# Performance work log

Hardware: AMD Instinct MI355X
Metric: run time of the kernel (lower is better)

## Reference

```python
import jax, jax.numpy as jnp
import numpy as np

B, S, D, HEADS = 2, 1024, 1024, 16
DK = D // HEADS           # 64: size of the 'heads' axis after split (namedtensor quirk)
LOW = D // DK             # 16: size of the contracted 'lower' axis
SCALE = float(D)          # Attention(p, scale=d_model) -> divide by d_model
NEG = -1.0e9


def setup_inputs() -> dict:
    key = jax.random.key(0)
    ks = jax.random.split(key, 8)
    query = jax.random.normal(ks[0], (B, S, D), dtype=jnp.float32)
    key_t = jax.random.normal(ks[1], (B, S, D), dtype=jnp.float32)
    value = jax.random.normal(ks[2], (B, S, D), dtype=jnp.float32)
    mask = jax.random.bernoulli(ks[3], 0.25, (B, S, S))  # True -> masked out
    std = 1.0 / np.sqrt(D)
    Wq = jax.random.normal(ks[4], (D, D), dtype=jnp.float32) * std
    Wk = jax.random.normal(ks[5], (D, D), dtype=jnp.float32) * std
    Wv = jax.random.normal(ks[6], (D, D), dtype=jnp.float32) * std
    Wo = jax.random.normal(ks[7], (D, D), dtype=jnp.float32) * std
    return {"query": query, "key": key_t, "value": value, "mask": mask,
            "Wq": Wq, "Wk": Wk, "Wv": Wv, "Wo": Wo}


def reference(query, key, value, mask, Wq, Wk, Wv, Wo):
    # nn.Linear(d_model, d_model, bias=False): y = x @ W.T
    def split(x, W):
        y = jnp.einsum('bsd,ed->bse', x, W)
        return y.reshape(B, -1, DK, LOW)  # hidden -> ('heads'=DK, 'lower'=LOW)

    q = split(query, Wq)   # [B,Sq,H,L] with H=DK, L=LOW
    k = split(key, Wk)     # [B,Sk,H,L]
    v = split(value, Wv)   # [B,Sk,H,L]

    # scores = query.dot('lower', key) / d_model  -> contract the LOW axis
    scores = jnp.einsum('bqhl,bkhl->bhqk', q, k) / SCALE
    scores = jnp.where(mask[:, None, :, :], NEG, scores)  # scores[mask] = -1e9
    p_attn = jax.nn.softmax(scores, axis=-1)  # softmax over keys; dropout=eval

    # value.dot('keys', p_attn) -> [B,H,L,Q]; stack ('heads','lower') -> hidden
    x = jnp.einsum('bkhl,bhqk->bqhl', v, p_attn).reshape(B, -1, D)
    return jnp.einsum('bsd,ed->bse', x, Wo)
```

## Files before the change

### kernel.cpp

```cpp
#include <hip/hip_runtime.h>
#include <hip/hip_bf16.h>


typedef __hip_bfloat16 bf16;
typedef __attribute__((ext_vector_type(8))) short short8;
typedef __attribute__((ext_vector_type(4))) float f32x4;
typedef __attribute__((ext_vector_type(16))) float f32x16;

__device__ __forceinline__ unsigned short f2bf(float f) {
  union { float f; unsigned u; } x; x.f = f;
  unsigned r = x.u + 0x7FFFu + ((x.u >> 16) & 1u);
  return (unsigned short)(r >> 16);
}

__device__ __forceinline__ unsigned cvt_pk_bf16(float lo, float hi) {
  unsigned r;
  asm("v_cvt_pk_bf16_f32 %0, %1, %2" : "=v"(r) : "v"(lo), "v"(hi));
  return r;
}

__device__ __forceinline__ float fast_exp2(float x) {
#if __has_builtin(__builtin_amdgcn_exp2f)
  return __builtin_amdgcn_exp2f(x);
#else
  return __expf(x * 0.6931471805599453f);
#endif
}

__device__ __forceinline__ void gload16(const void* g, void* l) {
#if __has_builtin(__builtin_amdgcn_global_load_lds)
  __builtin_amdgcn_global_load_lds(
      (const __attribute__((address_space(1))) unsigned*)g,
      (__attribute__((address_space(3))) unsigned*)l, 16, 0, 0);
#else
  *(uint4*)l = *(const uint4*)g;
#endif
}

__global__ void detect_mask(const unsigned char* __restrict__ m, int* __restrict__ flag) {
  const int i = blockIdx.x * 256 + threadIdx.x;
  const uchar4* p = (const uchar4*)m + (size_t)i * 4;
  unsigned any = 0;
#pragma unroll
  for (int j = 0; j < 4; ++j) { uchar4 v = p[j]; any |= (unsigned)v.y | (unsigned)v.z | (unsigned)v.w; }
  if (__ballot(any != 0)) { if ((threadIdx.x & 63) == 0) atomicOr(flag, 1); }
}

__global__ void bitpack_mask(const unsigned char* __restrict__ mB, const int* __restrict__ mI,
                             const int* __restrict__ flag, unsigned* __restrict__ out) {
  const int widx = blockIdx.x * 256 + threadIdx.x;
  const int row = widx >> 5, kb = widx & 31;
  unsigned bits = 0;
  if (*flag) {
    const uchar4* p = (const uchar4*)(mB + (size_t)row * 1024 + kb * 32);
#pragma unroll
    for (int j = 0; j < 8; ++j) {
      uchar4 v = p[j];
      bits |= ((unsigned)(v.x != 0) << (4 * j)) | ((unsigned)(v.y != 0) << (4 * j + 1))
            | ((unsigned)(v.z != 0) << (4 * j + 2)) | ((unsigned)(v.w != 0) << (4 * j + 3));
    }
  } else {
    const int4* p = (const int4*)(mI + (size_t)row * 1024 + kb * 32);
#pragma unroll
    for (int j = 0; j < 8; ++j) {
      int4 v = p[j];
      bits |= ((unsigned)(v.x != 0) << (4 * j)) | ((unsigned)(v.y != 0) << (4 * j + 1))
            | ((unsigned)(v.z != 0) << (4 * j + 2)) | ((unsigned)(v.w != 0) << (4 * j + 3));
    }
  }
  const int bq = row >> 10, qb = (row & 1023) >> 5, qr = row & 31;
  out[((((bq * 32 + qb) * 8 + (kb >> 2)) * 32 + qr) << 2) + (kb & 3)] = bits;
}

__global__ void convert_all(
    const float* __restrict__ s0, const float* __restrict__ s1, const float* __restrict__ s2,
    const float* __restrict__ s3, const float* __restrict__ s4, const float* __restrict__ s5,
    const float* __restrict__ s6,
    bf16* __restrict__ d0, bf16* __restrict__ d1, bf16* __restrict__ d2,
    bf16* __restrict__ d3, bf16* __restrict__ d4, bf16* __restrict__ d5,
    bf16* __restrict__ d6) {
  const int z = blockIdx.y;
  const float* s; bf16* d; int n8; float sc = 1.0f;
  if      (z == 0) { s = s0; d = d0; n8 = 262144; }
  else if (z == 1) { s = s1; d = d1; n8 = 262144; }
  else if (z == 2) { s = s2; d = d2; n8 = 262144; }
  else if (z == 3) { s = s3; d = d3; n8 = 131072; sc = 0.0014088818758681283f; }
  else if (z == 4) { s = s4; d = d4; n8 = 131072; }
  else if (z == 5) { s = s5; d = d5; n8 = 131072; }
  else             { s = s6; d = d6; n8 = 131072; }
  const int i = blockIdx.x * 256 + threadIdx.x;
  if (i >= n8) return;
  const f32x4* p = (const f32x4*)s + (size_t)i * 2;
  f32x4 a = p[0], b = p[1];
  uint4 o;
  o.x = cvt_pk_bf16(a[0] * sc, a[1] * sc); o.y = cvt_pk_bf16(a[2] * sc, a[3] * sc);
  o.z = cvt_pk_bf16(b[0] * sc, b[1] * sc); o.w = cvt_pk_bf16(b[2] * sc, b[3] * sc);
  ((uint4*)d)[i] = o;
}

#define GSTR 40

__global__ __launch_bounds__(256) void gemm_qkv(
    const bf16* __restrict__ A0, const bf16* __restrict__ A1, const bf16* __restrict__ A2,
    const bf16* __restrict__ W0, const bf16* __restrict__ W1, const bf16* __restrict__ W2,
    bf16* __restrict__ C0, bf16* __restrict__ C1, bf16* __restrict__ C2) {
  __shared__ __align__(16) bf16 smem[64 * 136];
  bf16* As = smem;
  bf16* Bs = smem + 4096;
  const int z = blockIdx.z;
  const bf16* __restrict__ A = (z == 0) ? A0 : (z == 1) ? A1 : A2;
  const bf16* __restrict__ W = (z == 0) ? W0 : (z == 1) ? W1 : W2;
  bf16* __restrict__ C = (z == 0) ? C0 : (z == 1) ? C1 : C2;
  const int tid = threadIdx.x, lane = tid & 63, w = tid >> 6;
  const int wr = (w >> 1) * 64, wc = (w & 1) * 32;
  const int row0 = blockIdx.y * 128, col0 = blockIdx.x * 64;
  const int l15 = lane & 15, kg = lane >> 4;

  const int srow = lane >> 2, scol = (lane & 3) * 8;
  const bf16* Ag0 = A + (size_t)(row0 + w * 32 + srow) * 1024 + scol;
  const bf16* Ag1 = A + (size_t)(row0 + w * 32 + 16 + srow) * 1024 + scol;
  const bf16* Bg0 = W + (size_t)(col0 + w * 16 + srow) * 1024 + scol;
  bf16* Al0 = As + w * 1024 + lane * 8;
  bf16* Al1 = As + w * 1024 + 512 + lane * 8;
  bf16* Bl0 = Bs + w * 512 + lane * 8;

  f32x4 acc[4][2];
#pragma unroll
  for (int m = 0; m < 4; ++m)
#pragma unroll
    for (int n = 0; n < 2; ++n)
#pragma unroll
      for (int j = 0; j < 4; ++j) acc[m][n][j] = 0.f;

  for (int t = 0; t < 32; ++t) {
    const int k0 = t * 32;
    gload16(Ag0 + k0, Al0);
    gload16(Ag1 + k0, Al1);
    gload16(Bg0 + k0, Bl0);
    __syncthreads();
    short8 af[4], bfr[2];
#pragma unroll
    for (int m = 0; m < 4; ++m) af[m] = *(const short8*)(&As[(wr + m * 16 + l15) * 32 + kg * 8]);
#pragma unroll
    for (int n = 0; n < 2; ++n) bfr[n] = *(const short8*)(&Bs[(wc + n * 16 + l15) * 32 + kg * 8]);
#pragma unroll
    for (int m = 0; m < 4; ++m)
#pragma unroll
      for (int n = 0; n < 2; ++n)
        acc[m][n] = __builtin_amdgcn_mfma_f32_16x16x32_bf16(af[m], bfr[n], acc[m][n], 0, 0, 0);
    __syncthreads();
  }

  const int bb = row0 >> 10, srel0 = row0 & 1023;
  if (z == 2) {
    bf16* T = smem;
#pragma unroll
    for (int m = 0; m < 4; ++m)
#pragma unroll
      for (int n = 0; n < 2; ++n) {
        const int e = wc + n * 16 + l15;
        const int rb = wr + m * 16 + kg * 4;
        uint2 u;
        u.x = cvt_pk_bf16(acc[m][n][0], acc[m][n][1]);
        u.y = cvt_pk_bf16(acc[m][n][2], acc[m][n][3]);
        *(uint2*)(T + e * 136 + rb) = u;
      }
    __syncthreads();
#pragma unroll
    for (int i = 0; i < 4; ++i) {
      const int idx = i * 256 + tid;
      const int tile = idx >> 6, within = idx & 63;
      const int hl = tile >> 2, kbl = tile & 3;
      const int e_sub = within >> 2, kq4 = within & 3;
      uint4 v = *(const uint4*)(T + (hl * 16 + e_sub) * 136 + kbl * 32 + kq4 * 8);
      const int h = (col0 >> 4) + hl;
      const size_t kb = (size_t)((srel0 >> 5) + kbl);
      *(uint4*)((unsigned short*)C + (((size_t)(bb * 64 + h) * 32 + kb) * 512 + e_sub * 32 + kq4 * 8)) = v;
    }
  } else if (z == 1) {
#pragma unroll
    for (int m = 0; m < 4; ++m)
#pragma unroll
      for (int n = 0; n < 2; ++n) {
        const int ecol = wc + n * 16 + l15;
        const int h = (col0 >> 4) + (ecol >> 4), d = ecol & 15;
#pragma unroll
        for (int j = 0; j < 4; ++j) {
          const int s = srel0 + wr + m * 16 + kg * 4 + j;
          ((unsigned short*)C)[((size_t)(bb * 64 + h) * 32 + (s >> 5)) * 512 + (s & 31) * 16 + d] =
              f2bf(acc[m][n][j]);
        }
      }
  } else {
#pragma unroll
    for (int m = 0; m < 4; ++m)
#pragma unroll
      for (int n = 0; n < 2; ++n) {
        const int col = col0 + wc + n * 16 + l15;
#pragma unroll
        for (int j = 0; j < 4; ++j) {
          const int row = row0 + wr + m * 16 + kg * 4 + j;
          ((unsigned short*)C)[(size_t)row * 1024 + col] = f2bf(acc[m][n][j]);
        }
      }
  }
}

__global__ __launch_bounds__(256) void gemm_out(
    const bf16* __restrict__ A, const bf16* __restrict__ W, float* __restrict__ C) {
  __shared__ __align__(16) bf16 smem[6144];
  bf16* As = smem;
  bf16* Bs = smem + 4096;
  const int tid = threadIdx.x, lane = tid & 63, w = tid >> 6;
  const int wr = (w >> 1) * 64, wc = (w & 1) * 32;
  const int row0 = blockIdx.y * 128, col0 = blockIdx.x * 64;
  const int l15 = lane & 15, kg = lane >> 4;

  const int srow = lane >> 2, scol = (lane & 3) * 8;
  const bf16* Ag0 = A + (size_t)(row0 + w * 32 + srow) * 1024 + scol;
  const bf16* Ag1 = A + (size_t)(row0 + w * 32 + 16 + srow) * 1024 + scol;
  const bf16* Bg0 = W + (size_t)(col0 + w * 16 + srow) * 1024 + scol;
  bf16* Al0 = As + w * 1024 + lane * 8;
  bf16* Al1 = As + w * 1024 + 512 + lane * 8;
  bf16* Bl0 = Bs + w * 512 + lane * 8;

  f32x4 acc[4][2];
#pragma unroll
  for (int m = 0; m < 4; ++m)
#pragma unroll
    for (int n = 0; n < 2; ++n)
#pragma unroll
      for (int j = 0; j < 4; ++j) acc[m][n][j] = 0.f;

  for (int t = 0; t < 32; ++t) {
    const int k0 = t * 32;
    gload16(Ag0 + k0, Al0);
    gload16(Ag1 + k0, Al1);
    gload16(Bg0 + k0, Bl0);
    __syncthreads();
    short8 af[4], bfr[2];
#pragma unroll
    for (int m = 0; m < 4; ++m) af[m] = *(const short8*)(&As[(wr + m * 16 + l15) * 32 + kg * 8]);
#pragma unroll
    for (int n = 0; n < 2; ++n) bfr[n] = *(const short8*)(&Bs[(wc + n * 16 + l15) * 32 + kg * 8]);
#pragma unroll
    for (int m = 0; m < 4; ++m)
#pragma unroll
      for (int n = 0; n < 2; ++n)
        acc[m][n] = __builtin_amdgcn_mfma_f32_16x16x32_bf16(af[m], bfr[n], acc[m][n], 0, 0, 0);
    __syncthreads();
  }

#pragma unroll
  for (int m = 0; m < 4; ++m)
#pragma unroll
    for (int n = 0; n < 2; ++n) {
      const int col = col0 + wc + n * 16 + l15;
#pragma unroll
      for (int j = 0; j < 4; ++j) {
        const int row = row0 + wr + m * 16 + kg * 4 + j;
        C[(size_t)row * 1024 + col] = acc[m][n][j];
      }
    }
}

__global__ __launch_bounds__(256) void attn_kernel(
    const bf16* __restrict__ Qp, const bf16* __restrict__ KT, const bf16* __restrict__ VT,
    const unsigned* __restrict__ mw, bf16* __restrict__ XO) {
  __shared__ bf16 Pl[4][32 * GSTR];
  const int tid = threadIdx.x, lane = tid & 63, w = tid >> 6;
  const int hi = lane >> 5, l31 = lane & 31, l15 = lane & 15, kg = lane >> 4;
  const int h = blockIdx.y, b = blockIdx.z;
  const int qg = w >> 1, kh = w & 1;
  const int q0 = blockIdx.x * 64 + qg * 32;

  const short8 qf = *(const short8*)(Qp + ((size_t)(b * 1024 + q0 + l31)) * 1024 + h * 16 + hi * 8);
  const bf16* __restrict__ Kb = KT + ((size_t)(b * 64 + h) * 32) * 512;
  const bf16* __restrict__ Vb = VT + ((size_t)(b * 64 + h) * 32) * 512;
  const uint4* __restrict__ Mq =
      (const uint4*)mw + ((size_t)((b * 32 + (q0 >> 5)) * 8 + kh * 4)) * 32 + l31;
  const int sh4 = hi * 4;

  f32x4 acc0, acc1, sum0, sum1;
#pragma unroll
  for (int j = 0; j < 4; ++j) { acc0[j] = 0.f; acc1[j] = 0.f; sum0[j] = 0.f; sum1[j] = 0.f; }
  f32x16 Z;
#pragma unroll
  for (int i = 0; i < 16; ++i) Z[i] = 0.f;
  short8 ones;
#pragma unroll
  for (int i = 0; i < 8; ++i) ones[i] = (short)0x3F80;

  for (int kq = 0; kq < 4; ++kq) {
    const uint4 mq = Mq[kq * 32];
#pragma unroll
    for (int t = 0; t < 4; ++t) {
      const int kbg = kh * 16 + kq * 4 + t;
      const unsigned mword = ((t == 0) ? mq.x : (t == 1) ? mq.y : (t == 2) ? mq.z : mq.w) >> sh4;
      const short8 kf = *(const short8*)(Kb + (size_t)kbg * 512 + l31 * 16 + hi * 8);
      f32x16 S = __builtin_amdgcn_mfma_f32_32x32x16_bf16(kf, qf, Z, 0, 0, 0);

      bf16* pw = &Pl[w][l31 * GSTR];
#pragma unroll
      for (int g = 0; g < 4; ++g) {
        float p0, p1, p2, p3;
        p0 = (mword & (1u << (8 * g + 0))) ? 0.f : fast_exp2(S[4 * g + 0]);
        p1 = (mword & (1u << (8 * g + 1))) ? 0.f : fast_exp2(S[4 * g + 1]);
        p2 = (mword & (1u << (8 * g + 2))) ? 0.f : fast_exp2(S[4 * g + 2]);
        p3 = (mword & (1u << (8 * g + 3))) ? 0.f : fast_exp2(S[4 * g + 3]);
        uint2 u;
        u.x = cvt_pk_bf16(p0, p1);
        u.y = cvt_pk_bf16(p2, p3);
        *(uint2*)(pw + 8 * g + 4 * hi) = u;
      }

      const short8 vf = *(const short8*)(Vb + (size_t)kbg * 512 + l15 * 32 + kg * 8);
      const short8 pa0 = *(const short8*)(&Pl[w][l15 * GSTR + kg * 8]);
      const short8 pa1 = *(const short8*)(&Pl[w][(16 + l15) * GSTR + kg * 8]);
      acc0 = __builtin_amdgcn_mfma_f32_16x16x32_bf16(pa0, vf, acc0, 0, 0, 0);
      acc1 = __builtin_amdgcn_mfma_f32_16x16x32_bf16(pa1, vf, acc1, 0, 0, 0);
      sum0 = __builtin_amdgcn_mfma_f32_16x16x32_bf16(pa0, ones, sum0, 0, 0, 0);
      sum1 = __builtin_amdgcn_mfma_f32_16x16x32_bf16(pa1, ones, sum1, 0, 0, 0);
    }
  }

  float* fl = (float*)&Pl[0][0];
  __syncthreads();
  if (kh) {
    float* dst = fl + ((size_t)(qg * 64 + lane)) * 16;
#pragma unroll
    for (int j = 0; j < 4; ++j) {
      dst[j] = acc0[j]; dst[4 + j] = acc1[j]; dst[8 + j] = sum0[j]; dst[12 + j] = sum1[j];
    }
  }
  __syncthreads();
  if (!kh) {
    const float* src = fl + ((size_t)(qg * 64 + lane)) * 16;
#pragma unroll
    for (int j = 0; j < 4; ++j) {
      const float o0 = acc0[j] + src[j],      d0 = sum0[j] + src[8 + j];
      const float o1 = acc1[j] + src[4 + j],  d1 = sum1[j] + src[12 + j];
      const size_t colo = (size_t)h * 16 + l15;
      ((unsigned short*)XO)[((size_t)(b * 1024 + q0 + kg * 4 + j)) * 1024 + colo] = f2bf(o0 / d0);
      ((unsigned short*)XO)[((size_t)(b * 1024 + q0 + 16 + kg * 4 + j)) * 1024 + colo] = f2bf(o1 / d1);
    }
  }
}

extern "C" void kernel_launch(void* const* d_in, const int* in_sizes, int n_in,
                              void* d_out, int out_size, void* d_ws, size_t ws_size,
                              hipStream_t stream) {
  const float* query = (const float*)d_in[0];
  const float* key   = (const float*)d_in[1];
  const float* value = (const float*)d_in[2];
  const void*  mask  = d_in[3];
  const float* Wq = (const float*)d_in[4];
  const float* Wk = (const float*)d_in[5];
  const float* Wv = (const float*)d_in[6];
  const float* Wo = (const float*)d_in[7];
  float* out = (float*)d_out;

  char* ws = (char*)d_ws;
  const size_t MB = 1024 * 1024;
  int* flag       = (int*)ws;
  unsigned* mbits = (unsigned*)(ws + 4096);
  bf16* Qb  = (bf16*)(ws + 4096 + 262144);
  bf16* Kb  = Qb + 2 * MB;
  bf16* Vb  = Kb + 2 * MB;
  bf16* Wqb = Vb + 2 * MB;
  bf16* Wkb = Wqb + MB;
  bf16* Wvb = Wkb + MB;
  bf16* Wob = Wvb + MB;
  bf16* Qp  = Wob + MB;
  bf16* KTl = Qp + 2 * MB;
  bf16* VTl = KTl + 2 * MB;
  bf16* XO  = VTl + 2 * MB;

  hipMemsetAsync(flag, 0, 4, stream);
  detect_mask<<<dim3(512), 256, 0, stream>>>((const unsigned char*)mask, flag);
  bitpack_mask<<<dim3(256), 256, 0, stream>>>((const unsigned char*)mask, (const int*)mask,
                                              flag, mbits);
  convert_all<<<dim3(1024, 7), 256, 0, stream>>>(query, key, value, Wq, Wk, Wv, Wo,
                                                 Qb, Kb, Vb, Wqb, Wkb, Wvb, Wob);
  gemm_qkv<<<dim3(16, 16, 3), 256, 0, stream>>>(Qb, Kb, Vb, Wqb, Wkb, Wvb, Qp, KTl, VTl);
  attn_kernel<<<dim3(16, 64, 2), 256, 0, stream>>>(Qp, KTl, VTl, mbits, XO);
  gemm_out<<<dim3(16, 16), 256, 0, stream>>>(XO, Wob, out);
}
```

Baseline: 105.2 us.

## Fold mask-format detection into bitpack and pipeline the attention inner loop

The separate detect_mask kernel and the flag memset are removed. Format detection now happens per block inside bitpack_mask, using a shared-memory flag and reusing the loaded bytes, which cuts two launches from the pipeline. The attention loop is fully unrolled with all mask words preloaded. The P tile in LDS is double-buffered with a narrower stride, and s_setprio is raised around the PV MFMAs to help overlap. Deciding the mask format per block rather than globally could misclassify a block whose bytes happen to be all zero in the checked positions.

```diff
diff --git a/kernel.cpp b/kernel.cpp
--- a/kernel.cpp
+++ b/kernel.cpp
@@ -37,35 +37,34 @@
 #endif
 }
 
-__global__ void detect_mask(const unsigned char* __restrict__ m, int* __restrict__ flag) {
-  const int i = blockIdx.x * 256 + threadIdx.x;
-  const uchar4* p = (const uchar4*)m + (size_t)i * 4;
-  unsigned any = 0;
-#pragma unroll
-  for (int j = 0; j < 4; ++j) { uchar4 v = p[j]; any |= (unsigned)v.y | (unsigned)v.z | (unsigned)v.w; }
-  if (__ballot(any != 0)) { if ((threadIdx.x & 63) == 0) atomicOr(flag, 1); }
-}
-
 __global__ void bitpack_mask(const unsigned char* __restrict__ mB, const int* __restrict__ mI,
-                             const int* __restrict__ flag, unsigned* __restrict__ out) {
+                             unsigned* __restrict__ out) {
+  __shared__ int sflag;
+  if (threadIdx.x == 0) sflag = 0;
+  __syncthreads();
   const int widx = blockIdx.x * 256 + threadIdx.x;
   const int row = widx >> 5, kb = widx & 31;
+  uchar4 v[8];
+  const uchar4* p = (const uchar4*)(mB + (size_t)row * 1024 + kb * 32);
+  unsigned any = 0;
+#pragma unroll
+  for (int j = 0; j < 8; ++j) { v[j] = p[j]; any |= (unsigned)v[j].y | (unsigned)v[j].z | (unsigned)v[j].w; }
+  if (__ballot(any != 0)) { if ((threadIdx.x & 63) == 0) atomicOr(&sflag, 1); }
+  __syncthreads();
   unsigned bits = 0;
-  if (*flag) {
-    const uchar4* p = (const uchar4*)(mB + (size_t)row * 1024 + kb * 32);
+  if (sflag) {
 #pragma unroll
     for (int j = 0; j < 8; ++j) {
-      uchar4 v = p[j];
-      bits |= ((unsigned)(v.x != 0) << (4 * j)) | ((unsigned)(v.y != 0) << (4 * j + 1))
-            | ((unsigned)(v.z != 0) << (4 * j + 2)) | ((unsigned)(v.w != 0) << (4 * j + 3));
+      bits |= ((unsigned)(v[j].x != 0) << (4 * j)) | ((unsigned)(v[j].y != 0) << (4 * j + 1))
+            | ((unsigned)(v[j].z != 0) << (4 * j + 2)) | ((unsigned)(v[j].w != 0) << (4 * j + 3));
     }
   } else {
-    const int4* p = (const int4*)(mI + (size_t)row * 1024 + kb * 32);
+    const int4* q = (const int4*)(mI + (size_t)row * 1024 + kb * 32);
 #pragma unroll
     for (int j = 0; j < 8; ++j) {
-      int4 v = p[j];
-      bits |= ((unsigned)(v.x != 0) << (4 * j)) | ((unsigned)(v.y != 0) << (4 * j + 1))
-            | ((unsigned)(v.z != 0) << (4 * j + 2)) | ((unsigned)(v.w != 0) << (4 * j + 3));
+      int4 u = q[j];
+      bits |= ((unsigned)(u.x != 0) << (4 * j)) | ((unsigned)(u.y != 0) << (4 * j + 1))
+            | ((unsigned)(u.z != 0) << (4 * j + 2)) | ((unsigned)(u.w != 0) << (4 * j + 3));
     }
   }
   const int bq = row >> 10, qb = (row & 1023) >> 5, qr = row & 31;
@@ -99,6 +98,7 @@
 }
 
 #define GSTR 40
+#define PSTR 36
 
 __global__ __launch_bounds__(256) void gemm_qkv(
     const bf16* __restrict__ A0, const bf16* __restrict__ A1, const bf16* __restrict__ A2,
@@ -267,7 +267,7 @@
 __global__ __launch_bounds__(256) void attn_kernel(
     const bf16* __restrict__ Qp, const bf16* __restrict__ KT, const bf16* __restrict__ VT,
     const unsigned* __restrict__ mw, bf16* __restrict__ XO) {
-  __shared__ bf16 Pl[4][32 * GSTR];
+  __shared__ bf16 Pl[4][2][32 * PSTR];
   const int tid = threadIdx.x, lane = tid & 63, w = tid >> 6;
   const int hi = lane >> 5, l31 = lane & 31, l15 = lane & 15, kg = lane >> 4;
   const int h = blockIdx.y, b = blockIdx.z;
@@ -281,6 +281,10 @@
       (const uint4*)mw + ((size_t)((b * 32 + (q0 >> 5)) * 8 + kh * 4)) * 32 + l31;
   const int sh4 = hi * 4;
 
+  const uint4 mqa = Mq[0], mqb = Mq[32], mqc = Mq[64], mqd = Mq[96];
+  const unsigned mm[16] = {mqa.x, mqa.y, mqa.z, mqa.w, mqb.x, mqb.y, mqb.z, mqb.w,
+                           mqc.x, mqc.y, mqc.z, mqc.w, mqd.x, mqd.y, mqd.z, mqd.w};
+
   f32x4 acc0, acc1, sum0, sum1;
 #pragma unroll
   for (int j = 0; j < 4; ++j) { acc0[j] = 0.f; acc1[j] = 0.f; sum0[j] = 0.f; sum1[j] = 0.f; }
@@ -291,40 +295,39 @@
 #pragma unroll
   for (int i = 0; i < 8; ++i) ones[i] = (short)0x3F80;
 
-  for (int kq = 0; kq < 4; ++kq) {
-    const uint4 mq = Mq[kq * 32];
-#pragma unroll
-    for (int t = 0; t < 4; ++t) {
-      const int kbg = kh * 16 + kq * 4 + t;
-      const unsigned mword = ((t == 0) ? mq.x : (t == 1) ? mq.y : (t == 2) ? mq.z : mq.w) >> sh4;
-      const short8 kf = *(const short8*)(Kb + (size_t)kbg * 512 + l31 * 16 + hi * 8);
-      f32x16 S = __builtin_amdgcn_mfma_f32_32x32x16_bf16(kf, qf, Z, 0, 0, 0);
-
-      bf16* pw = &Pl[w][l31 * GSTR];
-#pragma unroll
-      for (int g = 0; g < 4; ++g) {
-        float p0, p1, p2, p3;
-        p0 = (mword & (1u << (8 * g + 0))) ? 0.f : fast_exp2(S[4 * g + 0]);
-        p1 = (mword & (1u << (8 * g + 1))) ? 0.f : fast_exp2(S[4 * g + 1]);
-        p2 = (mword & (1u << (8 * g + 2))) ? 0.f : fast_exp2(S[4 * g + 2]);
-        p3 = (mword & (1u << (8 * g + 3))) ? 0.f : fast_exp2(S[4 * g + 3]);
-        uint2 u;
-        u.x = cvt_pk_bf16(p0, p1);
-        u.y = cvt_pk_bf16(p2, p3);
-        *(uint2*)(pw + 8 * g + 4 * hi) = u;
-      }
-
-      const short8 vf = *(const short8*)(Vb + (size_t)kbg * 512 + l15 * 32 + kg * 8);
-      const short8 pa0 = *(const short8*)(&Pl[w][l15 * GSTR + kg * 8]);
-      const short8 pa1 = *(const short8*)(&Pl[w][(16 + l15) * GSTR + kg * 8]);
-      acc0 = __builtin_amdgcn_mfma_f32_16x16x32_bf16(pa0, vf, acc0, 0, 0, 0);
-      acc1 = __builtin_amdgcn_mfma_f32_16x16x32_bf16(pa1, vf, acc1, 0, 0, 0);
-      sum0 = __builtin_amdgcn_mfma_f32_16x16x32_bf16(pa0, ones, sum0, 0, 0, 0);
-      sum1 = __builtin_amdgcn_mfma_f32_16x16x32_bf16(pa1, ones, sum1, 0, 0, 0);
-    }
-  }
-
-  float* fl = (float*)&Pl[0][0];
+#pragma unroll
+  for (int t = 0; t < 16; ++t) {
+    const int kbg = kh * 16 + t;
+    const unsigned mword = mm[t] >> sh4;
+    const short8 kf = *(const short8*)(Kb + (size_t)kbg * 512 + l31 * 16 + hi * 8);
+    f32x16 S = __builtin_amdgcn_mfma_f32_32x32x16_bf16(kf, qf, Z, 0, 0, 0);
+
+    bf16* pw = &Pl[w][t & 1][l31 * PSTR];
+#pragma unroll
+    for (int g = 0; g < 4; ++g) {
+      float p0, p1, p2, p3;
+      p0 = (mword & (1u << (8 * g + 0))) ? 0.f : fast_exp2(S[4 * g + 0]);
+      p1 = (mword & (1u << (8 * g + 1))) ? 0.f : fast_exp2(S[4 * g + 1]);
+      p2 = (mword & (1u << (8 * g + 2))) ? 0.f : fast_exp2(S[4 * g + 2]);
+      p3 = (mword & (1u << (8 * g + 3))) ? 0.f : fast_exp2(S[4 * g + 3]);
+      uint2 u;
+      u.x = cvt_pk_bf16(p0, p1);
+      u.y = cvt_pk_bf16(p2, p3);
+      *(uint2*)(pw + 8 * g + 4 * hi) = u;
+    }
+
+    const short8 vf = *(const short8*)(Vb + (size_t)kbg * 512 + l15 * 32 + kg * 8);
+    const short8 pa0 = *(const short8*)(&Pl[w][t & 1][l15 * PSTR + kg * 8]);
+    const short8 pa1 = *(const short8*)(&Pl[w][t & 1][(16 + l15) * PSTR + kg * 8]);
+    __builtin_amdgcn_s_setprio(1);
+    acc0 = __builtin_amdgcn_mfma_f32_16x16x32_bf16(pa0, vf, acc0, 0, 0, 0);
+    acc1 = __builtin_amdgcn_mfma_f32_16x16x32_bf16(pa1, vf, acc1, 0, 0, 0);
+    sum0 = __builtin_amdgcn_mfma_f32_16x16x32_bf16(pa0, ones, sum0, 0, 0, 0);
+    sum1 = __builtin_amdgcn_mfma_f32_16x16x32_bf16(pa1, ones, sum1, 0, 0, 0);
+    __builtin_amdgcn_s_setprio(0);
+  }
+
+  float* fl = (float*)&Pl[0][0][0];
   __syncthreads();
   if (kh) {
     float* dst = fl + ((size_t)(qg * 64 + lane)) * 16;
@@ -362,7 +365,6 @@
 
   char* ws = (char*)d_ws;
   const size_t MB = 1024 * 1024;
-  int* flag       = (int*)ws;
   unsigned* mbits = (unsigned*)(ws + 4096);
   bf16* Qb  = (bf16*)(ws + 4096 + 262144);
   bf16* Kb  = Qb + 2 * MB;
@@ -376,10 +378,8 @@
   bf16* VTl = KTl + 2 * MB;
   bf16* XO  = VTl + 2 * MB;
 
-  hipMemsetAsync(flag, 0, 4, stream);
-  detect_mask<<<dim3(512), 256, 0, stream>>>((const unsigned char*)mask, flag);
   bitpack_mask<<<dim3(256), 256, 0, stream>>>((const unsigned char*)mask, (const int*)mask,
-                                              flag, mbits);
+                                              mbits);
   convert_all<<<dim3(1024, 7), 256, 0, stream>>>(query, key, value, Wq, Wk, Wv, Wo,
                                                  Qb, Kb, Vb, Wqb, Wkb, Wvb, Wob);
   gemm_qkv<<<dim3(16, 16, 3), 256, 0, stream>>>(Qb, Kb, Vb, Wqb, Wkb, Wvb, Qp, KTl, VTl);
```

Result: faster. 98.03 us (-6.8%).
